# Kernel optimization log

Measured on AMD Instinct MI355X. Metric: run time of the kernel, lower is better.

Reference implementation:

```python
import jax, jax.numpy as jnp
import numpy as np

NUM_CLASSES = 80
SCORE_THR = 0.2
NMS_THR = 0.3
MAX_PER_IMAGE = 100
TOPK_PER_CLASS = 100  # cap on pre-NMS candidates per (image, class); >= max_per_image
ANCHOR_MASK = [[6, 7, 8], [3, 4, 5], [0, 1, 2]]
COCO_ANCHORS = np.array([[10, 13], [16, 30], [33, 23], [30, 61], [62, 45],
                         [59, 119], [116, 90], [156, 198], [373, 326]], dtype=np.float32)


def yolo_head(feats, layer_anchors, num_classes, input_shape):
    # feats: [B, 3*(5+C), gh, gw]
    B = feats.shape[0]
    gh, gw = feats.shape[2], feats.shape[3]
    na = layer_anchors.shape[0]
    f = feats.reshape(B, na, num_classes + 5, gh, gw).transpose(0, 3, 4, 1, 2)  # [B,gh,gw,3,5+C]
    gy, gx = jnp.meshgrid(jnp.arange(gh), jnp.arange(gw), indexing='ij')
    grid = jnp.stack([gx, gy], axis=-1).astype(f.dtype)[None, :, :, None, :]  # [1,gh,gw,1,2]
    # literal translation: divide by tensor([gh, gw]) (square grids in practice)
    box_xy = (jax.nn.sigmoid(f[..., :2]) + grid) / jnp.array([gh, gw], f.dtype)
    box_wh = jnp.exp(f[..., 2:4]) * layer_anchors[None, None, None, :, :] / input_shape[None, None, None, None, :]
    conf = jax.nn.sigmoid(f[..., 4:5])
    probs = jax.nn.sigmoid(f[..., 5:])
    return box_xy, box_wh, conf, probs


def yolo_correct_boxes(box_xy, box_wh, input_shape, image_shape):
    box_yx = box_xy[..., ::-1]
    box_hw = box_wh[..., ::-1]
    new_shape = jnp.round(image_shape * jnp.min(input_shape / image_shape))
    offset = (input_shape - new_shape) / 2.0 / input_shape
    scale = input_shape / new_shape
    box_yx = (box_yx - offset) * scale
    box_hw = box_hw * scale
    mins = box_yx - box_hw / 2.0
    maxes = box_yx + box_hw / 2.0
    boxes = jnp.concatenate([mins, maxes], axis=-1)  # (ymin, xmin, ymax, xmax)
    return boxes * jnp.concatenate([image_shape, image_shape])


def decode_layer(feats, layer_anchors, input_shape, image_shape):
    box_xy, box_wh, conf, probs = yolo_head(feats, layer_anchors, NUM_CLASSES, input_shape)
    boxes = yolo_correct_boxes(box_xy, box_wh, input_shape, image_shape)  # [B,gh,gw,3,4]
    B = feats.shape[0]
    return boxes.reshape(B, -1, 4), (conf * probs).reshape(B, -1, NUM_CLASSES)


def pairwise_iou(b):
    # b: [K,4] (y1,x1,y2,x2)
    y1, x1, y2, x2 = b[:, 0], b[:, 1], b[:, 2], b[:, 3]
    area = jnp.maximum(y2 - y1, 0) * jnp.maximum(x2 - x1, 0)
    iy1 = jnp.maximum(y1[:, None], y1[None, :])
    ix1 = jnp.maximum(x1[:, None], x1[None, :])
    iy2 = jnp.minimum(y2[:, None], y2[None, :])
    ix2 = jnp.minimum(x2[:, None], x2[None, :])
    inter = jnp.maximum(iy2 - iy1, 0) * jnp.maximum(ix2 - ix1, 0)
    return inter / (area[:, None] + area[None, :] - inter + 1e-9)


def greedy_nms(boxes, valid):
    # boxes [K,4] sorted by descending score; valid [K] bool. Returns keep mask [K].
    K = boxes.shape[0]
    iou = jax.lax.stop_gradient(pairwise_iou(boxes))
    idx = jnp.arange(K)
    def body(i, sup):
        keep_i = valid[i] & (~sup[i])
        return sup | (keep_i & (iou[i] > NMS_THR) & (idx > i))
    sup = jax.lax.fori_loop(0, K, body, jnp.zeros((K,), bool))
    return valid & (~sup)


def setup_inputs() -> dict:
    key = jax.random.key(0)
    k0, k1, k2 = jax.random.split(key, 3)
    B, F = 16, 3 * (5 + NUM_CLASSES)
    feat0 = jax.random.normal(k0, (B, F, 19, 19), jnp.float32)
    feat1 = jax.random.normal(k1, (B, F, 38, 38), jnp.float32)
    feat2 = jax.random.normal(k2, (B, F, 76, 76), jnp.float32)
    anchors = jnp.asarray(COCO_ANCHORS)
    image_shape = jnp.array([480.0, 640.0], jnp.float32)
    return {"feat0": feat0, "feat1": feat1, "feat2": feat2,
            "anchors": anchors, "image_shape": image_shape}


def reference(feat0, feat1, feat2, anchors, image_shape):
    input_shape = jnp.array([feat0.shape[2] * 32, feat0.shape[3] * 32], jnp.float32)
    feats = [feat0, feat1, feat2]
    boxes_l, scores_l = [], []
    for l in range(3):
        b, s = decode_layer(feats[l], anchors[np.array(ANCHOR_MASK[l])], input_shape, image_shape)
        boxes_l.append(b)
        scores_l.append(s)
    boxes = jnp.concatenate(boxes_l, axis=1)    # [B,N,4]
    scores = jnp.concatenate(scores_l, axis=1)  # [B,N,C]
    B = scores.shape[0]
    sc = scores.transpose(0, 2, 1)              # [B,C,N]
    top_s, top_i = jax.lax.top_k(sc, TOPK_PER_CLASS)              # [B,C,K]
    top_b = jnp.take_along_axis(boxes[:, None, :, :], top_i[..., None], axis=2)  # [B,C,K,4]
    valid = top_s >= SCORE_THR
    keep = jax.vmap(jax.vmap(greedy_nms))(top_b, valid)           # [B,C,K]
    cand = jnp.where(keep, top_s, -1.0)
    flat_s = cand.reshape(B, -1)                 # [B, C*K]
    flat_b = top_b.reshape(B, -1, 4)
    sel_s, sel_i = jax.lax.top_k(flat_s, MAX_PER_IMAGE)           # [B,100]
    sel_b = jnp.take_along_axis(flat_b, sel_i[..., None], axis=1)  # [B,100,4]
    sel_c = (sel_i // TOPK_PER_CLASS).astype(jnp.float32)
    # dets: (ymin, xmin, ymax, xmax, score, class); score == -1 marks padding
    return jnp.concatenate([sel_b, sel_s[..., None], sel_c[..., None]], axis=-1)
```

## Files before the change

kernel.cpp:

```cpp
#include <hip/hip_runtime.h>


#define NTOT   22743
#define NCLS   80
#define TOPK   100
#define KPAD   22752
#define NG2    2166
#define Q_L1   17328
#define Q_L0   21660
#define SCORE_THR 0.2f
#define NMS_THR   0.3f

__device__ __forceinline__ float sig_exact(float x) {
    return 1.0f / (1.0f + expf(-x));
}
__device__ __forceinline__ float sig_fast(float x) {
    return __builtin_amdgcn_rcpf(1.0f + __expf(-x));
}
__device__ __forceinline__ unsigned pack2(float cfa, float lga, float cfb, float lgb) {
    unsigned ka = __float_as_uint(cfa * sig_fast(lga)) >> 16;
    unsigned kb = __float_as_uint(cfb * sig_fast(lgb)) >> 16;
    return ka | (kb << 16);
}

__global__ __launch_bounds__(256) void k_decode(
    const float* __restrict__ f0, const float* __restrict__ f1,
    const float* __restrict__ f2, const float* __restrict__ anchors,
    const float* __restrict__ imshape, float4* __restrict__ boxes,
    float* __restrict__ conf_q, int total) {
    int gid = blockIdx.x * 256 + threadIdx.x;
    if (gid >= total) return;
    int b = gid / NTOT; int p = gid - b * NTOT;

    const float* f; int ghw, gw, l, off, a, s;
    if (p < 1083)      { f=f0; off=0;    ghw=361;  gw=19; l=0; int r=p;      a=r/361;  s=r-a*361;  }
    else if (p < 5415) { f=f1; off=1083; ghw=1444; gw=38; l=1; int r=p-1083; a=r/1444; s=r-a*1444; }
    else               { f=f2; off=5415; ghw=5776; gw=76; l=2; int r=p-5415; a=r/5776; s=r-a*5776; }
    int y = s / gw, x = s - y * gw;

    const float* q = f + ((size_t)(b * 255 + a * 85) * ghw + s);
    float tx = q[0], ty = q[ghw], tw = q[2*ghw], th = q[3*ghw], tc = q[4*ghw];

    int arow = (2 - l) * 3 + a;
    float aw = anchors[arow * 2], ah = anchors[arow * 2 + 1];
    float imh = imshape[0], imw = imshape[1];
    float gf = (float)gw;

    float bxx = (sig_exact(tx) + (float)x) / gf;
    float bxy = (sig_exact(ty) + (float)y) / gf;
    float bw  = expf(tw) * aw / 608.0f;
    float bh  = expf(th) * ah / 608.0f;

    float r  = fminf(608.0f / imh, 608.0f / imw);
    float nh = rintf(imh * r), nw = rintf(imw * r);
    float offy = (608.0f - nh) / 2.0f / 608.0f;
    float offx = (608.0f - nw) / 2.0f / 608.0f;
    float scy = 608.0f / nh, scx = 608.0f / nw;

    float cy = (bxy - offy) * scy;
    float cx = (bxx - offx) * scx;
    float hh = bh * scy, ww = bw * scx;

    int n = off + 3 * s + a;
    boxes[(size_t)b * NTOT + n] =
        make_float4((cy - hh / 2.0f) * imh, (cx - ww / 2.0f) * imw,
                    (cy + hh / 2.0f) * imh, (cx + ww / 2.0f) * imw);
    int qi = (l == 2) ? (a * 5776 + s)
           : (l == 1) ? (Q_L1 + a * 1444 + s)
                      : (Q_L0 + a * 361 + s);
    conf_q[(size_t)b * KPAD + qi] = sig_exact(tc);
}

__device__ void find_pivot(unsigned* hist, int H, unsigned target,
                           unsigned* suf, unsigned* sh_p, unsigned* sh_above) {
    const int tid = threadIdx.x;
    const int per = H >> 8;
    if (tid < 256) {
        unsigned acc = 0;
        for (int u = 0; u < per; ++u) acc += hist[tid * per + u];
        suf[tid] = acc;
    }
    __syncthreads();
    for (int off = 1; off < 256; off <<= 1) {
        unsigned v = 0;
        if (tid < 256) v = (tid + off < 256) ? suf[tid + off] : 0u;
        __syncthreads();
        if (tid < 256) suf[tid] += v;
        __syncthreads();
    }
    if (tid < 256) {
        unsigned mysuf = suf[tid];
        unsigned nxt = (tid == 255) ? 0u : suf[tid + 1];
        if (mysuf >= target && nxt < target) {
            unsigned above = nxt;
            for (int h = tid * per + per - 1; h >= tid * per; --h) {
                unsigned c2 = above + hist[h];
                if (c2 >= target) { *sh_p = (unsigned)h; *sh_above = above; break; }
                above = c2;
            }
        }
    }
    __syncthreads();
}

__device__ __forceinline__ void collect_cand(
    int b, int c, int q, const float* __restrict__ f0,
    const float* __restrict__ f1, const float* __restrict__ f2,
    const float* __restrict__ conf_q, unsigned long long* buf,
    unsigned* sh_cnt) {
    int a, s, nbase, ghw;
    const float* f;
    if (q < Q_L1)      { a = q / 5776;  s = q - a * 5776;  f = f2; ghw = 5776; nbase = 5415; }
    else if (q < Q_L0) { int r = q - Q_L1; a = r / 1444; s = r - a * 1444; f = f1; ghw = 1444; nbase = 1083; }
    else               { int r = q - Q_L0; a = r / 361;  s = r - a * 361;  f = f0; ghw = 361;  nbase = 0;    }
    float t  = f[((size_t)(b * 255 + a * 85 + 5 + c)) * ghw + s];
    float cf = conf_q[(size_t)b * KPAD + q];
    float sce = cf * sig_exact(t);
    int n = nbase + 3 * s + a;
    unsigned slot = atomicAdd(sh_cnt, 1u);
    if (slot < 512)
        buf[slot] = (((unsigned long long)__float_as_uint(sce)) << 32)
                    | (unsigned)(~n);
}

__device__ __forceinline__ void hist8(unsigned* histp, unsigned w0, unsigned w1,
                                      unsigned w2, unsigned w3) {
    unsigned ks[8] = { w0 & 0xFFFFu, w0 >> 16, w1 & 0xFFFFu, w1 >> 16,
                       w2 & 0xFFFFu, w2 >> 16, w3 & 0xFFFFu, w3 >> 16 };
    #pragma unroll
    for (int j = 0; j < 8; ++j)
        atomicAdd(&histp[ks[j] >> 2], 1u << (((ks[j] >> 1) & 1u) * 16));
}

__global__ __launch_bounds__(512, 4) void k_topk(
    const float* __restrict__ f0, const float* __restrict__ f1,
    const float* __restrict__ f2, const float* __restrict__ conf_q,
    const float4* __restrict__ boxes, float4* __restrict__ top_b,
    float* __restrict__ cand) {
    __shared__ unsigned int histp[4096];
    __shared__ unsigned long long buf[512];
    __shared__ unsigned int wsum[4];
    __shared__ float sb_y1[TOPK], sb_x1[TOPK], sb_y2[TOPK], sb_x2[TOPK], sb_s[TOPK];
    __shared__ unsigned int sh_p, sh_cnt;

    const int tid = threadIdx.x;
    const int row = blockIdx.x;
    const int b = row / NCLS, c = row - b * NCLS;
    const float* cq = conf_q + (size_t)b * KPAD;

    for (int i = tid; i < 4096; i += 512) histp[i] = 0;
    if (tid == 0) sh_cnt = 0;
    __syncthreads();

    uint4 v[5];
    bool  val[5];
    #pragma unroll
    for (int k = 0; k < 5; ++k) {
        int g = tid + k * 512;
        val[k] = (g < NG2);
        if (val[k]) {
            int q = g * 8;
            int a = q / 5776, s = q - a * 5776;
            const float* fp = f2 + ((size_t)(b * 255 + a * 85 + 5 + c)) * 5776 + s;
            float4 l0 = *(const float4*)fp;
            float4 l1 = *(const float4*)(fp + 4);
            float4 c0 = *(const float4*)(cq + q);
            float4 c1 = *(const float4*)(cq + q + 4);
            v[k].x = pack2(c0.x, l0.x, c0.y, l0.y);
            v[k].y = pack2(c0.z, l0.z, c0.w, l0.w);
            v[k].z = pack2(c1.x, l1.x, c1.y, l1.y);
            v[k].w = pack2(c1.z, l1.z, c1.w, l1.w);
            hist8(histp, v[k].x, v[k].y, v[k].z, v[k].w);
        } else v[k] = make_uint4(0, 0, 0, 0);
    }

    const bool lv = (tid < 361);
    unsigned k1p[6];
    if (lv) {
        #pragma unroll
        for (int p = 0; p < 3; ++p) {
            const float* fp = f1 + ((size_t)(b * 255 + p * 85 + 5 + c)) * 1444 + 4 * tid;
            float4 lg = *(const float4*)fp;
            float4 cf = *(const float4*)(cq + Q_L1 + p * 1444 + 4 * tid);
            unsigned w0 = pack2(cf.x, lg.x, cf.y, lg.y);
            unsigned w1 = pack2(cf.z, lg.z, cf.w, lg.w);
            k1p[2*p] = w0; k1p[2*p+1] = w1;
            unsigned ks[4] = { w0 & 0xFFFFu, w0 >> 16, w1 & 0xFFFFu, w1 >> 16 };
            #pragma unroll
            for (int j = 0; j < 4; ++j)
                atomicAdd(&histp[ks[j] >> 2], 1u << (((ks[j] >> 1) & 1u) * 16));
        }
    }

    unsigned k0[3];
    if (lv) {
        #pragma unroll
        for (int p = 0; p < 3; ++p) {
            float g0 = f0[((size_t)(b * 255 + p * 85 + 5 + c)) * 361 + tid];
            float c0 = cq[Q_L0 + p * 361 + tid];
            k0[p] = __float_as_uint(c0 * sig_fast(g0)) >> 16;
            atomicAdd(&histp[k0[p] >> 2], 1u << (((k0[p] >> 1) & 1u) * 16));
        }
    }
    __syncthreads();

    {
        const int lane = tid & 63;
        unsigned own = 0;
        if (tid < 256) {
            #pragma unroll
            for (int u = 0; u < 16; ++u) {
                unsigned w = histp[tid * 16 + u];
                own += (w & 0xFFFFu) + (w >> 16);
            }
        }
        unsigned acc = own;
        #pragma unroll
        for (int d = 1; d < 64; d <<= 1) {
            unsigned vv = __shfl_down(acc, d, 64);
            if (lane + d < 64) acc += vv;
        }
        if (tid < 256 && lane == 0) wsum[tid >> 6] = acc;
        __syncthreads();
        if (tid < 256) {
            unsigned tail = 0;
            for (int w2 = (tid >> 6) + 1; w2 < 4; ++w2) tail += wsum[w2];
            unsigned suft = acc + tail;
            unsigned nxt  = suft - own;
            if (suft >= TOPK && nxt < TOPK) {
                unsigned above = nxt;
                for (int bb = 31; bb >= 0; --bb) {
                    unsigned w = histp[tid * 16 + (bb >> 1)];
                    unsigned cnt = (bb & 1) ? (w >> 16) : (w & 0xFFFFu);
                    if (above + cnt >= TOPK) { sh_p = (unsigned)(tid * 32 + bb); break; }
                    above += cnt;
                }
            }
        }
        __syncthreads();
    }
    const unsigned kthr = sh_p > 0 ? ((sh_p - 1) << 1) : 0u;

    #pragma unroll
    for (int k = 0; k < 5; ++k) if (val[k]) {
        unsigned ks[8] = { v[k].x & 0xFFFFu, v[k].x >> 16, v[k].y & 0xFFFFu, v[k].y >> 16,
                           v[k].z & 0xFFFFu, v[k].z >> 16, v[k].w & 0xFFFFu, v[k].w >> 16 };
        #pragma unroll
        for (int j = 0; j < 8; ++j)
            if (ks[j] >= kthr)
                collect_cand(b, c, (tid + k * 512) * 8 + j, f0, f1, f2, conf_q, buf, &sh_cnt);
    }
    if (lv) {
        #pragma unroll
        for (int p = 0; p < 3; ++p) {
            unsigned ks[4] = { k1p[2*p] & 0xFFFFu, k1p[2*p] >> 16,
                               k1p[2*p+1] & 0xFFFFu, k1p[2*p+1] >> 16 };
            #pragma unroll
            for (int j = 0; j < 4; ++j)
                if (ks[j] >= kthr)
                    collect_cand(b, c, Q_L1 + p * 1444 + 4 * tid + j, f0, f1, f2, conf_q, buf, &sh_cnt);
            if (k0[p] >= kthr)
                collect_cand(b, c, Q_L0 + p * 361 + tid, f0, f1, f2, conf_q, buf, &sh_cnt);
        }
    }
    __syncthreads();

    const int M = (int)min(sh_cnt, 512u);
    if (tid < M) {
        unsigned long long mykey = buf[tid];
        int rank = 0;
        for (int j = 0; j < M; ++j) rank += (buf[j] > mykey);
        if (rank < TOPK) {
            int n = (int)(~(unsigned)mykey);
            float4 bx = boxes[(size_t)b * NTOT + n];
            sb_y1[rank] = bx.x; sb_x1[rank] = bx.y;
            sb_y2[rank] = bx.z; sb_x2[rank] = bx.w;
            sb_s[rank]  = __uint_as_float((unsigned)(mykey >> 32));
            top_b[(size_t)row * TOPK + rank] = bx;
        }
    }
    __syncthreads();

    if (tid < 64) {
        const int j0 = tid, j1 = tid + 64;
        const bool v1 = (j1 < TOPK);
        float y10 = sb_y1[j0], x10 = sb_x1[j0], y20 = sb_y2[j0], x20 = sb_x2[j0];
        float s0 = sb_s[j0];
        float y11 = v1 ? sb_y1[j1] : 0.f, x11 = v1 ? sb_x1[j1] : 0.f;
        float y21 = v1 ? sb_y2[j1] : 0.f, x21 = v1 ? sb_x2[j1] : 0.f;
        float s1 = v1 ? sb_s[j1] : -1.0f;
        float ar0 = fmaxf(y20 - y10, 0.f) * fmaxf(x20 - x10, 0.f);
        float ar1 = fmaxf(y21 - y11, 0.f) * fmaxf(x21 - x11, 0.f);
        int sup0 = 0, sup1 = 0;
        for (int i = 0; i < TOPK; ++i) {
            float yi1 = sb_y1[i], xi1 = sb_x1[i], yi2 = sb_y2[i], xi2 = sb_x2[i];
            float si = sb_s[i];
            int supi = (i < 64) ? __shfl(sup0, i, 64) : __shfl(sup1, i - 64, 64);
            bool keep_i = (si >= SCORE_THR) && (supi == 0);
            if (keep_i) {
                float ari = fmaxf(yi2 - yi1, 0.f) * fmaxf(xi2 - xi1, 0.f);
                if (j0 > i) {
                    float ty1 = fmaxf(yi1, y10), tx1 = fmaxf(xi1, x10);
                    float ty2 = fminf(yi2, y20), tx2 = fminf(xi2, x20);
                    float inter = fmaxf(ty2 - ty1, 0.f) * fmaxf(tx2 - tx1, 0.f);
                    float iou = inter / (ari + ar0 - inter + 1e-9f);
                    if (iou > NMS_THR) sup0 = 1;
                }
                if (v1 && j1 > i) {
                    float ty1 = fmaxf(yi1, y11), tx1 = fmaxf(xi1, x11);
                    float ty2 = fminf(yi2, y21), tx2 = fminf(xi2, x21);
                    float inter = fmaxf(ty2 - ty1, 0.f) * fmaxf(tx2 - tx1, 0.f);
                    float iou = inter / (ari + ar1 - inter + 1e-9f);
                    if (iou > NMS_THR) sup1 = 1;
                }
            }
        }
        cand[(size_t)row * TOPK + j0] = (s0 >= SCORE_THR && sup0 == 0) ? s0 : -1.0f;
        if (v1)
            cand[(size_t)row * TOPK + j1] = (s1 >= SCORE_THR && sup1 == 0) ? s1 : -1.0f;
    }
}

__global__ __launch_bounds__(256) void k_final(
    const float* __restrict__ cand, const float4* __restrict__ top_b,
    float* __restrict__ out) {
    __shared__ float cs[8000];
    __shared__ unsigned int hist[4096];
    __shared__ unsigned long long buf[512];
    __shared__ unsigned int suf[256];
    __shared__ unsigned int sh_kp, sh_p1, sh_above1, sh_p2, sh_above2, sh_cnt;

    const int tid = threadIdx.x, b = blockIdx.x;
    if (tid == 0) { sh_kp = 0; sh_cnt = 0; }
    for (int i = tid; i < 4096; i += 256) hist[i] = 0;
    __syncthreads();

    unsigned lk = 0;
    for (int i = tid; i < 8000; i += 256) {
        float v = cand[b * 8000 + i];
        cs[i] = v;
        if (v > -0.5f) lk++;
    }
    atomicAdd(&sh_kp, lk);
    __syncthreads();
    unsigned Kp = sh_kp;

    if (Kp >= TOPK) {
        for (int i = tid; i < 8000; i += 256)
            if (cs[i] > -0.5f) atomicAdd(&hist[__float_as_uint(cs[i]) >> 19], 1u);
        __syncthreads();
        find_pivot(hist, 2048, TOPK, suf, &sh_p1, &sh_above1);
        unsigned p1 = sh_p1, above1 = sh_above1;
        for (int i = tid; i < 4096; i += 256) hist[i] = 0;
        __syncthreads();
        for (int i = tid; i < 8000; i += 256) {
            float v = cs[i];
            if (v > -0.5f) {
                unsigned bits = __float_as_uint(v);
                if ((bits >> 19) == p1) atomicAdd(&hist[(bits >> 7) & 0xFFFu], 1u);
            }
        }
        __syncthreads();
        find_pivot(hist, 4096, TOPK - above1, suf, &sh_p2, &sh_above2);
        unsigned p2 = sh_p2;
        for (int i = tid; i < 8000; i += 256) {
            float v = cs[i];
            if (v > -0.5f) {
                unsigned bits = __float_as_uint(v);
                unsigned b1 = bits >> 19;
                if (b1 > p1 || (b1 == p1 && ((bits >> 7) & 0xFFFu) >= p2)) {
                    unsigned slot = atomicAdd(&sh_cnt, 1u);
                    if (slot < 512)
                        buf[slot] = (((unsigned long long)bits) << 32) | (unsigned)(~i);
                }
            }
        }
    } else {
        for (int i = tid; i < 8000; i += 256) {
            float v = cs[i];
            if (v > -0.5f) {
                unsigned slot = atomicAdd(&sh_cnt, 1u);
                buf[slot] = (((unsigned long long)__float_as_uint(v)) << 32) | (unsigned)(~i);
            }
        }
        __syncthreads();
        if (tid == 0) {
            unsigned need = TOPK - Kp, got = 0;
            for (int i = 0; i < 8000 && got < need; ++i)
                if (cs[i] <= -0.5f) { buf[Kp + got] = (unsigned)(~i); got++; }
        }
    }
    __syncthreads();

    const int M2 = (Kp >= TOPK) ? (int)min(sh_cnt, 512u) : (int)TOPK;
    for (int i = tid; i < M2; i += 256) {
        unsigned long long key = buf[i];
        int rank = 0;
        for (int j = 0; j < M2; ++j) rank += (buf[j] > key);
        if (rank < TOPK) {
            int fi = (int)(~(unsigned)key);
            int c = fi / TOPK; int kk = fi - c * TOPK;
            float4 bb = top_b[((size_t)b * NCLS + c) * TOPK + kk];
            int base = (b * TOPK + rank) * 6;
            out[base + 0] = bb.x; out[base + 1] = bb.y;
            out[base + 2] = bb.z; out[base + 3] = bb.w;
            out[base + 4] = cs[fi]; out[base + 5] = (float)c;
        }
    }
}

extern "C" void kernel_launch(void* const* d_in, const int* in_sizes, int n_in,
                              void* d_out, int out_size, void* d_ws, size_t ws_size,
                              hipStream_t stream) {
    (void)n_in; (void)out_size; (void)ws_size;
    const float* f0      = (const float*)d_in[0];
    const float* f1      = (const float*)d_in[1];
    const float* f2      = (const float*)d_in[2];
    const float* anchors = (const float*)d_in[3];
    const float* imshape = (const float*)d_in[4];
    const int B = in_sizes[0] / (255 * 19 * 19);

    char* ws = (char*)d_ws;
    size_t o = 0;
    float4* boxes  = (float4*)(ws + o); o += (size_t)B * NTOT * sizeof(float4);
    float*  conf_q = (float*)(ws + o);  o += (size_t)B * KPAD * sizeof(float);
    float4* top_b  = (float4*)(ws + o); o += (size_t)B * NCLS * TOPK * sizeof(float4);
    float*  cand   = (float*)(ws + o);  o += (size_t)B * NCLS * TOPK * sizeof(float);
    float*  out    = (float*)d_out;

    const int total = B * NTOT;
    k_decode<<<(total + 255) / 256, 256, 0, stream>>>(f0, f1, f2, anchors, imshape,
                                                      boxes, conf_q, total);
    k_topk<<<B * NCLS, 512, 0, stream>>>(f0, f1, f2, conf_q, boxes,
                                         top_b, cand);
    k_final<<<B, 256, 0, stream>>>(cand, top_b, out);
}
```

Before: 247.4 us.

## Decode boxes lazily for top-k survivors and widen final selection block

The full decode pass that wrote a box for every anchor is replaced by a slim kernel that only computes objectness sigmoids into the conf buffer. Box coordinates are now decoded on demand inside the top-k kernel, only for the up to 100 winners per (image, class). This removes the boxes workspace write and read, at the cost of duplicated decode arithmetic across classes and scattered feature reads. The final per-image selection kernel also moves from 256 to 1024 threads to shorten its strided loops.

```diff
diff --git a/kernel.cpp b/kernel.cpp
--- a/kernel.cpp
+++ b/kernel.cpp
@@ -23,52 +23,18 @@
     return ka | (kb << 16);
 }
 
-__global__ __launch_bounds__(256) void k_decode(
+__global__ __launch_bounds__(256) void k_conf(
     const float* __restrict__ f0, const float* __restrict__ f1,
-    const float* __restrict__ f2, const float* __restrict__ anchors,
-    const float* __restrict__ imshape, float4* __restrict__ boxes,
-    float* __restrict__ conf_q, int total) {
+    const float* __restrict__ f2, float* __restrict__ conf_q, int total) {
     int gid = blockIdx.x * 256 + threadIdx.x;
     if (gid >= total) return;
-    int b = gid / NTOT; int p = gid - b * NTOT;
-
-    const float* f; int ghw, gw, l, off, a, s;
-    if (p < 1083)      { f=f0; off=0;    ghw=361;  gw=19; l=0; int r=p;      a=r/361;  s=r-a*361;  }
-    else if (p < 5415) { f=f1; off=1083; ghw=1444; gw=38; l=1; int r=p-1083; a=r/1444; s=r-a*1444; }
-    else               { f=f2; off=5415; ghw=5776; gw=76; l=2; int r=p-5415; a=r/5776; s=r-a*5776; }
-    int y = s / gw, x = s - y * gw;
-
-    const float* q = f + ((size_t)(b * 255 + a * 85) * ghw + s);
-    float tx = q[0], ty = q[ghw], tw = q[2*ghw], th = q[3*ghw], tc = q[4*ghw];
-
-    int arow = (2 - l) * 3 + a;
-    float aw = anchors[arow * 2], ah = anchors[arow * 2 + 1];
-    float imh = imshape[0], imw = imshape[1];
-    float gf = (float)gw;
-
-    float bxx = (sig_exact(tx) + (float)x) / gf;
-    float bxy = (sig_exact(ty) + (float)y) / gf;
-    float bw  = expf(tw) * aw / 608.0f;
-    float bh  = expf(th) * ah / 608.0f;
-
-    float r  = fminf(608.0f / imh, 608.0f / imw);
-    float nh = rintf(imh * r), nw = rintf(imw * r);
-    float offy = (608.0f - nh) / 2.0f / 608.0f;
-    float offx = (608.0f - nw) / 2.0f / 608.0f;
-    float scy = 608.0f / nh, scx = 608.0f / nw;
-
-    float cy = (bxy - offy) * scy;
-    float cx = (bxx - offx) * scx;
-    float hh = bh * scy, ww = bw * scx;
-
-    int n = off + 3 * s + a;
-    boxes[(size_t)b * NTOT + n] =
-        make_float4((cy - hh / 2.0f) * imh, (cx - ww / 2.0f) * imw,
-                    (cy + hh / 2.0f) * imh, (cx + ww / 2.0f) * imw);
-    int qi = (l == 2) ? (a * 5776 + s)
-           : (l == 1) ? (Q_L1 + a * 1444 + s)
-                      : (Q_L0 + a * 361 + s);
-    conf_q[(size_t)b * KPAD + qi] = sig_exact(tc);
+    int b = gid / NTOT; int q = gid - b * NTOT;
+    const float* f; int ghw, a, s;
+    if (q < Q_L1)      { f = f2; ghw = 5776; a = q / 5776;  s = q - a * 5776; }
+    else if (q < Q_L0) { f = f1; ghw = 1444; int r = q - Q_L1; a = r / 1444; s = r - a * 1444; }
+    else               { f = f0; ghw = 361;  int r = q - Q_L0; a = r / 361;  s = r - a * 361; }
+    float tc = f[((size_t)(b * 255 + a * 85 + 4)) * ghw + s];
+    conf_q[(size_t)b * KPAD + q] = sig_exact(tc);
 }
 
 __device__ void find_pivot(unsigned* hist, int H, unsigned target,
@@ -135,8 +101,8 @@
 __global__ __launch_bounds__(512, 4) void k_topk(
     const float* __restrict__ f0, const float* __restrict__ f1,
     const float* __restrict__ f2, const float* __restrict__ conf_q,
-    const float4* __restrict__ boxes, float4* __restrict__ top_b,
-    float* __restrict__ cand) {
+    const float* __restrict__ anchors, const float* __restrict__ imshape,
+    float4* __restrict__ top_b, float* __restrict__ cand) {
     __shared__ unsigned int histp[4096];
     __shared__ unsigned long long buf[512];
     __shared__ unsigned int wsum[4];
@@ -271,8 +237,34 @@
         int rank = 0;
         for (int j = 0; j < M; ++j) rank += (buf[j] > mykey);
         if (rank < TOPK) {
-            int n = (int)(~(unsigned)mykey);
-            float4 bx = boxes[(size_t)b * NTOT + n];
+            int nn = (int)(~(unsigned)mykey);
+            const float* f; int ghw, gw, l, off;
+            if (nn < 1083)      { f = f0; off = 0;    ghw = 361;  gw = 19; l = 0; }
+            else if (nn < 5415) { f = f1; off = 1083; ghw = 1444; gw = 38; l = 1; }
+            else                { f = f2; off = 5415; ghw = 5776; gw = 76; l = 2; }
+            int m2 = nn - off; int a = m2 % 3; int s = m2 / 3;
+            int y = s / gw, x = s - y * gw;
+            const float* qp = f + ((size_t)(b * 255 + a * 85)) * ghw + s;
+            float tx = qp[0], ty = qp[(size_t)ghw];
+            float tw = qp[2 * (size_t)ghw], th = qp[3 * (size_t)ghw];
+            int arow = (2 - l) * 3 + a;
+            float aw = anchors[arow * 2], ah = anchors[arow * 2 + 1];
+            float imh = imshape[0], imw = imshape[1];
+            float gf = (float)gw;
+            float bxx = (sig_exact(tx) + (float)x) / gf;
+            float bxy = (sig_exact(ty) + (float)y) / gf;
+            float bw  = expf(tw) * aw / 608.0f;
+            float bh  = expf(th) * ah / 608.0f;
+            float r  = fminf(608.0f / imh, 608.0f / imw);
+            float nh = rintf(imh * r), nw2 = rintf(imw * r);
+            float offy = (608.0f - nh) / 2.0f / 608.0f;
+            float offx = (608.0f - nw2) / 2.0f / 608.0f;
+            float scy = 608.0f / nh, scx = 608.0f / nw2;
+            float cy = (bxy - offy) * scy;
+            float cx = (bxx - offx) * scx;
+            float hh = bh * scy, ww = bw * scx;
+            float4 bx = make_float4((cy - hh / 2.0f) * imh, (cx - ww / 2.0f) * imw,
+                                    (cy + hh / 2.0f) * imh, (cx + ww / 2.0f) * imw);
             sb_y1[rank] = bx.x; sb_x1[rank] = bx.y;
             sb_y2[rank] = bx.z; sb_x2[rank] = bx.w;
             sb_s[rank]  = __uint_as_float((unsigned)(mykey >> 32));
@@ -321,7 +313,8 @@
     }
 }
 
-__global__ __launch_bounds__(256) void k_final(
+#define FBS 1024
+__global__ __launch_bounds__(FBS) void k_final(
     const float* __restrict__ cand, const float4* __restrict__ top_b,
     float* __restrict__ out) {
     __shared__ float cs[8000];
@@ -332,11 +325,11 @@
 
     const int tid = threadIdx.x, b = blockIdx.x;
     if (tid == 0) { sh_kp = 0; sh_cnt = 0; }
-    for (int i = tid; i < 4096; i += 256) hist[i] = 0;
+    for (int i = tid; i < 4096; i += FBS) hist[i] = 0;
     __syncthreads();
 
     unsigned lk = 0;
-    for (int i = tid; i < 8000; i += 256) {
+    for (int i = tid; i < 8000; i += FBS) {
         float v = cand[b * 8000 + i];
         cs[i] = v;
         if (v > -0.5f) lk++;
@@ -346,14 +339,14 @@
     unsigned Kp = sh_kp;
 
     if (Kp >= TOPK) {
-        for (int i = tid; i < 8000; i += 256)
+        for (int i = tid; i < 8000; i += FBS)
             if (cs[i] > -0.5f) atomicAdd(&hist[__float_as_uint(cs[i]) >> 19], 1u);
         __syncthreads();
         find_pivot(hist, 2048, TOPK, suf, &sh_p1, &sh_above1);
         unsigned p1 = sh_p1, above1 = sh_above1;
-        for (int i = tid; i < 4096; i += 256) hist[i] = 0;
-        __syncthreads();
-        for (int i = tid; i < 8000; i += 256) {
+        for (int i = tid; i < 4096; i += FBS) hist[i] = 0;
+        __syncthreads();
+        for (int i = tid; i < 8000; i += FBS) {
             float v = cs[i];
             if (v > -0.5f) {
                 unsigned bits = __float_as_uint(v);
@@ -363,7 +356,7 @@
         __syncthreads();
         find_pivot(hist, 4096, TOPK - above1, suf, &sh_p2, &sh_above2);
         unsigned p2 = sh_p2;
-        for (int i = tid; i < 8000; i += 256) {
+        for (int i = tid; i < 8000; i += FBS) {
             float v = cs[i];
             if (v > -0.5f) {
                 unsigned bits = __float_as_uint(v);
@@ -376,7 +369,7 @@
             }
         }
     } else {
-        for (int i = tid; i < 8000; i += 256) {
+        for (int i = tid; i < 8000; i += FBS) {
             float v = cs[i];
             if (v > -0.5f) {
                 unsigned slot = atomicAdd(&sh_cnt, 1u);
@@ -393,7 +386,7 @@
     __syncthreads();
 
     const int M2 = (Kp >= TOPK) ? (int)min(sh_cnt, 512u) : (int)TOPK;
-    for (int i = tid; i < M2; i += 256) {
+    for (int i = tid; i < M2; i += FBS) {
         unsigned long long key = buf[i];
         int rank = 0;
         for (int j = 0; j < M2; ++j) rank += (buf[j] > key);
@@ -422,16 +415,14 @@
 
     char* ws = (char*)d_ws;
     size_t o = 0;
-    float4* boxes  = (float4*)(ws + o); o += (size_t)B * NTOT * sizeof(float4);
     float*  conf_q = (float*)(ws + o);  o += (size_t)B * KPAD * sizeof(float);
     float4* top_b  = (float4*)(ws + o); o += (size_t)B * NCLS * TOPK * sizeof(float4);
     float*  cand   = (float*)(ws + o);  o += (size_t)B * NCLS * TOPK * sizeof(float);
     float*  out    = (float*)d_out;
 
     const int total = B * NTOT;
-    k_decode<<<(total + 255) / 256, 256, 0, stream>>>(f0, f1, f2, anchors, imshape,
-                                                      boxes, conf_q, total);
-    k_topk<<<B * NCLS, 512, 0, stream>>>(f0, f1, f2, conf_q, boxes,
+    k_conf<<<(total + 255) / 256, 256, 0, stream>>>(f0, f1, f2, conf_q, total);
+    k_topk<<<B * NCLS, 512, 0, stream>>>(f0, f1, f2, conf_q, anchors, imshape,
                                          top_b, cand);
-    k_final<<<B, 256, 0, stream>>>(cand, top_b, out);
-}
+    k_final<<<B, FBS, 0, stream>>>(cand, top_b, out);
+}
```

Measured after the change: 239.0 us (median of 2 runs). 3.4% less time.
